# Optimization experiments

Measured on AMD Instinct MI355X. Metric: run time of the kernel, lower is better.

The kernel has to match this reference:

```python
import jax, jax.numpy as jnp
import numpy as np

N_CG_ITERS = 100


def _conv_same(x, k):
    # x: [C,H,W], k: [kh,kw]; depthwise cross-correlation, zero padding ('same')
    C = x.shape[0]
    rhs = jnp.broadcast_to(k, (C, 1) + k.shape)  # [C,1,kh,kw]
    return jax.lax.conv_general_dilated(
        x[None], rhs, window_strides=(1, 1), padding='SAME',
        dimension_numbers=('NCHW', 'OIHW', 'NCHW'),
        feature_group_count=C)[0]


def _flip(k):
    return k[::-1, ::-1]


def _apply_A(p, kernel, wsq, reg_kernels):
    # A = K^T K + sum_i w_i^2 G_i^T G_i
    KtKp = _conv_same(_conv_same(p, kernel), _flip(kernel))
    def one_reg(g):
        return _conv_same(_conv_same(p, g), _flip(g))
    reg = jax.vmap(one_reg)(reg_kernels)  # [n_reg, C, H, W]
    return KtKp + jnp.einsum('n,nchw->chw', wsq, reg)


def setup_inputs() -> dict:
    key = jax.random.key(0)
    k1, k2, k3, k4 = jax.random.split(key, 4)
    image = jax.random.uniform(k1, (3, 512, 512), dtype=jnp.float32)
    kernel = jax.random.uniform(k2, (11, 11), dtype=jnp.float32)
    kernel = kernel / jnp.sum(kernel)  # normalized blur PSF
    reg_kernels = 0.01 * jax.random.normal(k3, (2, 3, 3), dtype=jnp.float32)
    reg_kernel_weights = 1.0 + 0.01 * jax.random.normal(k4, (2,), dtype=jnp.float32)
    return {'image': image, 'kernel': kernel,
            'reg_kernel_weights': reg_kernel_weights, 'reg_kernels': reg_kernels}


def reference(image, kernel, reg_kernel_weights, reg_kernels):
    wsq = reg_kernel_weights * reg_kernel_weights
    # CG init: b = K^T * image, x0 = image, r0 = b - A x0, p0 = r0
    b = _conv_same(image, _flip(kernel))
    x0 = image
    r0 = b - _apply_A(x0, kernel, wsq, reg_kernels)
    p0 = r0

    def cg_step(carry, _):
        x, r, p = carry
        Ap = _apply_A(p, kernel, wsq, reg_kernels)
        rTr = jnp.sum(r * r)
        alpha = rTr / jnp.sum(p * Ap)
        x_new = x + alpha * p
        r_new = r - alpha * Ap
        beta = jnp.sum(r_new * r_new) / rTr
        p_new = r_new + beta * p
        return (x_new, r_new, p_new), None

    (x, r, p), _ = jax.lax.scan(cg_step, (x0, r0, p0), None, length=N_CG_ITERS)
    return x  # xrp[0] -> solved image [C,H,W]
```

## Files before the change

kernel.cpp:

```cpp
#include <hip/hip_runtime.h>


static constexpr int H = 512, W = 512, CCH = 3;
static constexpr int TDIM = 64;
static constexpr int RAD = 5;
static constexpr int HALO = 10;
static constexpr int PR = TDIM + 2 * HALO;
static constexpr int PSTR = 84;
static constexpr int TR = TDIM + 2 * RAD;
static constexpr int TSTR = 76;
static constexpr int NBLK = CCH * 8 * 8;
static constexpr int NTHR = 512;
static constexpr int NITER = 100;
static constexpr int FRN = 2960;
static constexpr int SPN = 2160;

__device__ __forceinline__ void load18(const float* __restrict__ row, float* __restrict__ v)
{
    const float4 a = *reinterpret_cast<const float4*>(row + 0);
    const float4 b = *reinterpret_cast<const float4*>(row + 4);
    const float4 c = *reinterpret_cast<const float4*>(row + 8);
    const float4 d = *reinterpret_cast<const float4*>(row + 12);
    const float2 e = *reinterpret_cast<const float2*>(row + 16);
    v[0]=a.x; v[1]=a.y; v[2]=a.z; v[3]=a.w;
    v[4]=b.x; v[5]=b.y; v[6]=b.z; v[7]=b.w;
    v[8]=c.x; v[9]=c.y; v[10]=c.z; v[11]=c.w;
    v[12]=d.x; v[13]=d.y; v[14]=d.z; v[15]=d.w;
    v[16]=e.x; v[17]=e.y;
}

__device__ __forceinline__ float block_reduce0(float v, float* red, int tid)
{
    __syncthreads();
    #pragma unroll
    for (int m = 32; m; m >>= 1) v += __shfl_xor(v, m, 64);
    if ((tid & 63) == 0) red[tid >> 6] = v;
    __syncthreads();
    float s = 0.f;
    if (tid == 0) {
        #pragma unroll
        for (int i = 0; i < NTHR / 64; ++i) s += red[i];
    }
    return s;
}

__device__ __forceinline__ float allreduce_bar(unsigned long long* slots, unsigned seq,
                                               float thread_partial,
                                               float* red, float* bc, int tid, int bid)
{
    float part = block_reduce0(thread_partial, red, tid);
    asm volatile("s_waitcnt vmcnt(0)" ::: "memory");
    __syncthreads();
    unsigned long long* buf = slots + (size_t)(seq & 1u) * 256;
    if (tid == 0) {
        unsigned long long u = ((unsigned long long)seq << 32)
                             | (unsigned long long)__float_as_uint(part);
        __hip_atomic_store(&buf[bid], u, __ATOMIC_RELAXED, __HIP_MEMORY_SCOPE_AGENT);
    }
    float mine = 0.f;
    if (tid < NBLK) {
        unsigned long long v;
        for (;;) {
            v = __hip_atomic_load(&buf[tid], __ATOMIC_RELAXED, __HIP_MEMORY_SCOPE_AGENT);
            if ((unsigned)(v >> 32) == seq) break;
            __builtin_amdgcn_s_sleep(1);
        }
        mine = __uint_as_float((unsigned)v);
    }
    float s = block_reduce0(mine, red, tid);
    if (tid == 0) *bc = s;
    __syncthreads();
    return *bc;
}

__device__ __forceinline__ void conv_fwd_phase(const float* __restrict__ kern,
                                               const float* __restrict__ P_,
                                               float* __restrict__ T_,
                                               int by0, int bx0, int tid)
{
    for (int seg = tid; seg < TR * 10; seg += NTHR) {
        int chunk = seg / TR;
        int ry    = seg - chunk * TR;
        int rx0   = chunk << 3;
        int gy    = by0 - RAD + ry;
        bool rowIn = (gy >= 0 && gy < H);
        float acc[8];
        #pragma unroll
        for (int j = 0; j < 8; ++j) acc[j] = 0.f;
        for (int a = 0; a < 11; ++a) {
            float v[18];
            load18(P_ + (ry + a) * PSTR + rx0, v);
            #pragma unroll
            for (int b = 0; b < 11; ++b) {
                float kw = kern[a * 11 + b];
                #pragma unroll
                for (int j = 0; j < 8; ++j) acc[j] = fmaf(v[b + j], kw, acc[j]);
            }
        }
        #pragma unroll
        for (int j = 0; j < 8; ++j) {
            int gx = bx0 - RAD + rx0 + j;
            bool in = rowIn && gx >= 0 && gx < W;
            acc[j] = in ? acc[j] : 0.f;
        }
        float* dst = T_ + ry * TSTR + rx0;
        if (rx0 < 72) {
            *reinterpret_cast<float4*>(dst)     = make_float4(acc[0], acc[1], acc[2], acc[3]);
            *reinterpret_cast<float4*>(dst + 4) = make_float4(acc[4], acc[5], acc[6], acc[7]);
        } else {
            dst[0] = acc[0];
            dst[1] = acc[1];
        }
    }
}

__device__ __forceinline__ void conv11_flip_acc_v(const float* __restrict__ src, int stride,
                                                  int row0, int col0,
                                                  const float* __restrict__ kern,
                                                  float acc[8])
{
    for (int a = 0; a < 11; ++a) {
        float v[18];
        load18(src + (row0 + a) * stride + col0, v);
        #pragma unroll
        for (int b = 0; b < 11; ++b) {
            float kw = kern[(10 - a) * 11 + (10 - b)];
            #pragma unroll
            for (int j = 0; j < 8; ++j) acc[j] = fmaf(v[b + j], kw, acc[j]);
        }
    }
}

__device__ __forceinline__ void conv11_flip_acc_s(const float* __restrict__ src, int stride,
                                                  int row0, int col0,
                                                  const float* __restrict__ kern,
                                                  float acc[8])
{
    for (int a = 0; a < 11; ++a) {
        const float* row = src + (row0 + a) * stride + col0;
        float v[18];
        #pragma unroll
        for (int b = 0; b < 18; ++b) v[b] = row[b];
        #pragma unroll
        for (int b = 0; b < 11; ++b) {
            float kw = kern[(10 - a) * 11 + (10 - b)];
            #pragma unroll
            for (int j = 0; j < 8; ++j) acc[j] = fmaf(v[b + j], kw, acc[j]);
        }
    }
}

__device__ __forceinline__ void reg_acc(const float* __restrict__ P_,
                                        const float* __restrict__ CB_,
                                        const float* __restrict__ gk,
                                        float w0sq, float w1sq,
                                        int oy, int ox0, int gy, int gx0,
                                        float acc[8])
{
    bool interior = (gy >= 1 && gy < H - 1 && gx0 >= 1 && gx0 <= W - 9);
    if (interior) {
        for (int a = 0; a < 5; ++a) {
            const float* row = P_ + (oy + 8 + a) * PSTR + ox0 + 8;
            const float4 q0 = *reinterpret_cast<const float4*>(row);
            const float4 q1 = *reinterpret_cast<const float4*>(row + 4);
            const float4 q2 = *reinterpret_cast<const float4*>(row + 8);
            float v[12] = {q0.x,q0.y,q0.z,q0.w, q1.x,q1.y,q1.z,q1.w, q2.x,q2.y,q2.z,q2.w};
            #pragma unroll
            for (int b = 0; b < 5; ++b) {
                float cb = CB_[a * 5 + b];
                #pragma unroll
                for (int j = 0; j < 8; ++j) acc[j] = fmaf(v[b + j], cb, acc[j]);
            }
        }
    } else {
        for (int j = 0; j < 8; ++j) {
            int gx = gx0 + j;
            float racc = 0.f;
            for (int dy = -1; dy <= 1; ++dy)
                for (int dx = -1; dx <= 1; ++dx) {
                    int qy = gy + dy, qx = gx + dx;
                    if (qy >= 0 && qy < H && qx >= 0 && qx < W) {
                        float u0 = 0.f, u1 = 0.f;
                        int pr0 = oy + 10 + dy - 1, pc0 = ox0 + j + 10 + dx - 1;
                        for (int sy = 0; sy < 3; ++sy)
                            for (int sx = 0; sx < 3; ++sx) {
                                float pv = P_[(pr0 + sy) * PSTR + pc0 + sx];
                                u0 = fmaf(pv, gk[sy * 3 + sx], u0);
                                u1 = fmaf(pv, gk[9 + sy * 3 + sx], u1);
                            }
                        racc += w0sq * gk[(1 - dy) * 3 + (1 - dx)] * u0
                              + w1sq * gk[9 + (1 - dy) * 3 + (1 - dx)] * u1;
                    }
                }
            acc[j] += racc;
        }
    }
}

__global__ void slot_init(unsigned long long* slots) { slots[threadIdx.x] = 0ull; }

__global__ void __launch_bounds__(NTHR)
__attribute__((amdgpu_waves_per_eu(2, 2)))
deconv_cg(const float* __restrict__ img, const float* __restrict__ kern,
          const float* __restrict__ wts, const float* __restrict__ gk,
          float* __restrict__ out, float* __restrict__ ws)
{
    asm volatile("" ::: "v255");

    __shared__ alignas(16) float P[PR * PSTR + 8];
    __shared__ alignas(16) float T[TR * TSTR + 8];
    __shared__ float CB[25];
    __shared__ float red[NTHR / 64];
    __shared__ float bc;

    const int tid = threadIdx.x;
    const int bid = blockIdx.x;
    const int ch  = bid / 64;
    const int tt  = bid - ch * 64;
    const int by0 = (tt >> 3) * TDIM;
    const int bx0 = (tt & 7) * TDIM;

    const float* imgc = img + ch * H * W;
    unsigned long long* slots = (unsigned long long*)ws;
    float* Hc = ws + 1024 + (size_t)ch * H * W;

    const float w0 = wts[0], w1 = wts[1];
    const float w0sq = w0 * w0, w1sq = w1 * w1;

    if (tid < 25) {
        int ty = tid / 5 - 2, tx = tid % 5 - 2;
        float s = 0.f;
        for (int ay = 0; ay < 3; ++ay)
            for (int ax = 0; ax < 3; ++ax) {
                int by_ = ay + ty, bx_ = ax + tx;
                if (by_ >= 0 && by_ < 3 && bx_ >= 0 && bx_ < 3)
                    s += w0sq * gk[ay * 3 + ax] * gk[by_ * 3 + bx_]
                       + w1sq * gk[9 + ay * 3 + ax] * gk[9 + by_ * 3 + bx_];
            }
        CB[tid] = s;
    }

    const int oy  = tid & 63;
    const int ox0 = (tid >> 6) << 3;
    const int gy  = by0 + oy;
    const int gx0 = bx0 + ox0;

    int fP[6], fG[6];
    #pragma unroll
    for (int k = 0; k < 6; ++k) {
        int idx = tid + k * NTHR;
        fP[k] = -1; fG[k] = -1;
        if (idx < FRN) {
            int py, px;
            if (idx < 840)       { py = idx / 84;              px = idx - py * 84; }
            else if (idx < 1680) { int t = idx - 840;  py = 74 + t / 84; px = t - (t / 84) * 84; }
            else                 { int t = idx - 1680; py = 10 + t / 20;
                                   int c = t - (t / 20) * 20;  px = (c < 10) ? c : (c + 64); }
            int iy = by0 - HALO + py, ix = bx0 - HALO + px;
            if (iy >= 0 && iy < H && ix >= 0 && ix < W) {
                fP[k] = py * PSTR + px;
                fG[k] = iy * W + ix;
            }
        }
    }
    int pT[5], pG[5];
    #pragma unroll
    for (int k = 0; k < 5; ++k) {
        int idx = tid + k * NTHR;
        pT[k] = -1; pG[k] = 0;
        if (idx < SPN) {
            int sy, sx;
            if (idx < 640)       { sy = idx >> 6;              sx = idx & 63; }
            else if (idx < 1280) { int t = idx - 640;  sy = 54 + (t >> 6); sx = t & 63; }
            else                 { int t = idx - 1280; sy = 10 + t / 20;
                                   int c = t - (t / 20) * 20;  sx = (c < 10) ? c : (c + 44); }
            pT[k] = sy * TSTR + sx;
            pG[k] = (by0 + sy) * W + bx0 + sx;
        }
    }

    float xr[8], rr[8], pr[8];

    for (int idx = tid; idx < PR * PR; idx += NTHR) {
        int py = idx / PR, px = idx - py * PR;
        int iy = by0 - HALO + py, ix = bx0 - HALO + px;
        float v = 0.f;
        if (iy >= 0 && iy < H && ix >= 0 && ix < W) v = imgc[iy * W + ix];
        P[py * PSTR + px] = v;
    }
    __syncthreads();
    conv_fwd_phase(kern, P, T, by0, bx0, tid);
    __syncthreads();
    float rTr, beta = 0.f;
    {
        float accA[8], accB[8];
        #pragma unroll
        for (int j = 0; j < 8; ++j) { accA[j] = 0.f; accB[j] = 0.f; }
        conv11_flip_acc_v(T, TSTR, oy, ox0, kern, accA);
        conv11_flip_acc_s(P, PSTR, oy + 5, ox0 + 5, kern, accB);
        reg_acc(P, CB, gk, w0sq, w1sq, oy, ox0, gy, gx0, accA);
        float dr = 0.f;
        #pragma unroll
        for (int j = 0; j < 8; ++j) {
            float r0 = accB[j] - accA[j];
            rr[j] = r0;  pr[j] = r0;
            xr[j] = P[(oy + HALO) * PSTR + ox0 + HALO + j];
            dr = fmaf(r0, r0, dr);
        }
        __syncthreads();
        float* st = T + oy * TSTR + ox0;
        *reinterpret_cast<float4*>(st)     = make_float4(rr[0], rr[1], rr[2], rr[3]);
        *reinterpret_cast<float4*>(st + 4) = make_float4(rr[4], rr[5], rr[6], rr[7]);
        __syncthreads();
        #pragma unroll
        for (int k = 0; k < 5; ++k)
            if (pT[k] >= 0)
                __hip_atomic_store(&Hc[pG[k]], T[pT[k]],
                                   __ATOMIC_RELAXED, __HIP_MEMORY_SCOPE_AGENT);
        rTr = allreduce_bar(slots, 1u, dr, red, &bc, tid, bid);
    }

    for (int it = 0; it < NITER; ++it) {
        #pragma unroll
        for (int j = 0; j < 8; ++j) pr[j] = fmaf(beta, pr[j], rr[j]);
        float fv[6];
        #pragma unroll
        for (int k = 0; k < 6; ++k)
            fv[k] = (fG[k] >= 0)
                  ? __hip_atomic_load(&Hc[fG[k]], __ATOMIC_RELAXED, __HIP_MEMORY_SCOPE_AGENT)
                  : 0.f;
        #pragma unroll
        for (int k = 0; k < 6; ++k)
            if (fG[k] >= 0)
                P[fP[k]] = fmaf(beta, P[fP[k]], fv[k]);
        {
            float* ow = P + (oy + HALO) * PSTR + ox0 + HALO;
            *reinterpret_cast<float2*>(ow)     = make_float2(pr[0], pr[1]);
            *reinterpret_cast<float2*>(ow + 2) = make_float2(pr[2], pr[3]);
            *reinterpret_cast<float2*>(ow + 4) = make_float2(pr[4], pr[5]);
            *reinterpret_cast<float2*>(ow + 6) = make_float2(pr[6], pr[7]);
        }
        __syncthreads();

        conv_fwd_phase(kern, P, T, by0, bx0, tid);
        __syncthreads();

        float Ap[8];
        float dp = 0.f;
        {
            float acc[8];
            #pragma unroll
            for (int j = 0; j < 8; ++j) acc[j] = 0.f;
            conv11_flip_acc_v(T, TSTR, oy, ox0, kern, acc);
            reg_acc(P, CB, gk, w0sq, w1sq, oy, ox0, gy, gx0, acc);
            #pragma unroll
            for (int j = 0; j < 8; ++j) {
                Ap[j] = acc[j];
                dp = fmaf(pr[j], Ap[j], dp);
            }
        }
        float pAp   = allreduce_bar(slots, 2u * it + 2u, dp, red, &bc, tid, bid);
        float alpha = rTr / pAp;

        float dr = 0.f;
        #pragma unroll
        for (int j = 0; j < 8; ++j) {
            xr[j] = fmaf(alpha, pr[j], xr[j]);
            rr[j] = fmaf(-alpha, Ap[j], rr[j]);
            dr = fmaf(rr[j], rr[j], dr);
        }
        {
            float* st = T + oy * TSTR + ox0;
            *reinterpret_cast<float4*>(st)     = make_float4(rr[0], rr[1], rr[2], rr[3]);
            *reinterpret_cast<float4*>(st + 4) = make_float4(rr[4], rr[5], rr[6], rr[7]);
        }
        __syncthreads();
        #pragma unroll
        for (int k = 0; k < 5; ++k)
            if (pT[k] >= 0)
                __hip_atomic_store(&Hc[pG[k]], T[pT[k]],
                                   __ATOMIC_RELAXED, __HIP_MEMORY_SCOPE_AGENT);
        float s = allreduce_bar(slots, 2u * it + 3u, dr, red, &bc, tid, bid);
        beta = s / rTr;
        rTr  = s;
    }

    float* op = out + ch * H * W + gy * W + gx0;
    *reinterpret_cast<float4*>(op)     = make_float4(xr[0], xr[1], xr[2], xr[3]);
    *reinterpret_cast<float4*>(op + 4) = make_float4(xr[4], xr[5], xr[6], xr[7]);
}

extern "C" void kernel_launch(void* const* d_in, const int* in_sizes, int n_in,
                              void* d_out, int out_size, void* d_ws, size_t ws_size,
                              hipStream_t stream)
{
    (void)in_sizes; (void)n_in; (void)out_size; (void)ws_size;
    const float* img  = (const float*)d_in[0];
    const float* kern = (const float*)d_in[1];
    const float* wts  = (const float*)d_in[2];
    const float* gk   = (const float*)d_in[3];
    float* out = (float*)d_out;
    float* ws  = (float*)d_ws;

    slot_init<<<1, 512, 0, stream>>>((unsigned long long*)ws);
    deconv_cg<<<dim3(NBLK), dim3(NTHR), 0, stream>>>(img, kern, wts, gk, out, ws);
}
```

Baseline: 4.711 ms.

## Switch to Chronopoulos-Gear single-reduction CG with fused two-value grid allreduce

```diff
diff --git a/kernel.cpp b/kernel.cpp
--- a/kernel.cpp
+++ b/kernel.cpp
@@ -29,46 +29,57 @@
     v[16]=e.x; v[17]=e.y;
 }
 
-__device__ __forceinline__ float block_reduce0(float v, float* red, int tid)
+__device__ __forceinline__ float2 allreduce2_bar(unsigned long long* slots, unsigned seq,
+                                                 float va, float vb,
+                                                 float* redA, float* redB, float2* bc,
+                                                 int tid, int bid)
 {
     __syncthreads();
     #pragma unroll
-    for (int m = 32; m; m >>= 1) v += __shfl_xor(v, m, 64);
-    if ((tid & 63) == 0) red[tid >> 6] = v;
-    __syncthreads();
-    float s = 0.f;
+    for (int m = 32; m; m >>= 1) { va += __shfl_xor(va, m, 64); vb += __shfl_xor(vb, m, 64); }
+    if ((tid & 63) == 0) { redA[tid >> 6] = va; redB[tid >> 6] = vb; }
+    asm volatile("s_waitcnt vmcnt(0)" ::: "memory");
+    __syncthreads();
+    unsigned long long* bufA = slots + (size_t)(seq & 1u) * 512;
+    unsigned long long* bufB = bufA + 256;
     if (tid == 0) {
-        #pragma unroll
-        for (int i = 0; i < NTHR / 64; ++i) s += red[i];
-    }
-    return s;
-}
-
-__device__ __forceinline__ float allreduce_bar(unsigned long long* slots, unsigned seq,
-                                               float thread_partial,
-                                               float* red, float* bc, int tid, int bid)
-{
-    float part = block_reduce0(thread_partial, red, tid);
-    asm volatile("s_waitcnt vmcnt(0)" ::: "memory");
-    __syncthreads();
-    unsigned long long* buf = slots + (size_t)(seq & 1u) * 256;
-    if (tid == 0) {
-        unsigned long long u = ((unsigned long long)seq << 32)
-                             | (unsigned long long)__float_as_uint(part);
-        __hip_atomic_store(&buf[bid], u, __ATOMIC_RELAXED, __HIP_MEMORY_SCOPE_AGENT);
-    }
-    float mine = 0.f;
+        float sa = 0.f, sb = 0.f;
+        #pragma unroll
+        for (int i = 0; i < NTHR / 64; ++i) { sa += redA[i]; sb += redB[i]; }
+        __hip_atomic_store(&bufA[bid],
+            ((unsigned long long)seq << 32) | (unsigned long long)__float_as_uint(sa),
+            __ATOMIC_RELAXED, __HIP_MEMORY_SCOPE_AGENT);
+        __hip_atomic_store(&bufB[bid],
+            ((unsigned long long)seq << 32) | (unsigned long long)__float_as_uint(sb),
+            __ATOMIC_RELAXED, __HIP_MEMORY_SCOPE_AGENT);
+    }
+    float ma = 0.f, mb = 0.f;
     if (tid < NBLK) {
         unsigned long long v;
         for (;;) {
-            v = __hip_atomic_load(&buf[tid], __ATOMIC_RELAXED, __HIP_MEMORY_SCOPE_AGENT);
+            v = __hip_atomic_load(&bufA[tid], __ATOMIC_RELAXED, __HIP_MEMORY_SCOPE_AGENT);
             if ((unsigned)(v >> 32) == seq) break;
             __builtin_amdgcn_s_sleep(1);
         }
-        mine = __uint_as_float((unsigned)v);
-    }
-    float s = block_reduce0(mine, red, tid);
-    if (tid == 0) *bc = s;
+        ma = __uint_as_float((unsigned)v);
+        for (;;) {
+            v = __hip_atomic_load(&bufB[tid], __ATOMIC_RELAXED, __HIP_MEMORY_SCOPE_AGENT);
+            if ((unsigned)(v >> 32) == seq) break;
+            __builtin_amdgcn_s_sleep(1);
+        }
+        mb = __uint_as_float((unsigned)v);
+    }
+    __syncthreads();
+    #pragma unroll
+    for (int m = 32; m; m >>= 1) { ma += __shfl_xor(ma, m, 64); mb += __shfl_xor(mb, m, 64); }
+    if ((tid & 63) == 0) { redA[tid >> 6] = ma; redB[tid >> 6] = mb; }
+    __syncthreads();
+    if (tid == 0) {
+        float sa = 0.f, sb = 0.f;
+        #pragma unroll
+        for (int i = 0; i < NTHR / 64; ++i) { sa += redA[i]; sb += redB[i]; }
+        bc->x = sa; bc->y = sb;
+    }
     __syncthreads();
     return *bc;
 }
@@ -150,49 +161,47 @@
     }
 }
 
-__device__ __forceinline__ void reg_acc(const float* __restrict__ P_,
-                                        const float* __restrict__ CB_,
-                                        const float* __restrict__ gk,
-                                        float w0sq, float w1sq,
-                                        int oy, int ox0, int gy, int gx0,
-                                        float acc[8])
-{
-    bool interior = (gy >= 1 && gy < H - 1 && gx0 >= 1 && gx0 <= W - 9);
-    if (interior) {
-        for (int a = 0; a < 5; ++a) {
-            const float* row = P_ + (oy + 8 + a) * PSTR + ox0 + 8;
-            const float4 q0 = *reinterpret_cast<const float4*>(row);
-            const float4 q1 = *reinterpret_cast<const float4*>(row + 4);
-            const float4 q2 = *reinterpret_cast<const float4*>(row + 8);
-            float v[12] = {q0.x,q0.y,q0.z,q0.w, q1.x,q1.y,q1.z,q1.w, q2.x,q2.y,q2.z,q2.w};
-            #pragma unroll
-            for (int b = 0; b < 5; ++b) {
-                float cb = CB_[a * 5 + b];
-                #pragma unroll
-                for (int j = 0; j < 8; ++j) acc[j] = fmaf(v[b + j], cb, acc[j]);
-            }
-        }
-    } else {
+__device__ __forceinline__ void reg_uniform(const float* __restrict__ P_,
+                                            const float* __restrict__ CB_,
+                                            const float* __restrict__ gk,
+                                            float w0sq, float w1sq,
+                                            int oy, int ox0, int gy, int gx0,
+                                            float acc[8])
+{
+    for (int a = 0; a < 5; ++a) {
+        const float* row = P_ + (oy + 8 + a) * PSTR + ox0 + 8;
+        const float4 q0 = *reinterpret_cast<const float4*>(row);
+        const float4 q1 = *reinterpret_cast<const float4*>(row + 4);
+        const float4 q2 = *reinterpret_cast<const float4*>(row + 8);
+        float v[12] = {q0.x,q0.y,q0.z,q0.w, q1.x,q1.y,q1.z,q1.w, q2.x,q2.y,q2.z,q2.w};
+        #pragma unroll
+        for (int b = 0; b < 5; ++b) {
+            float cb = CB_[a * 5 + b];
+            #pragma unroll
+            for (int j = 0; j < 8; ++j) acc[j] = fmaf(v[b + j], cb, acc[j]);
+        }
+    }
+    if (!(gy > 0 && gy < H - 1 && gx0 > 0 && gx0 + 7 < W - 1)) {
         for (int j = 0; j < 8; ++j) {
             int gx = gx0 + j;
-            float racc = 0.f;
+            if (gy > 0 && gy < H - 1 && gx > 0 && gx < W - 1) continue;
+            float corr = 0.f;
             for (int dy = -1; dy <= 1; ++dy)
                 for (int dx = -1; dx <= 1; ++dx) {
                     int qy = gy + dy, qx = gx + dx;
-                    if (qy >= 0 && qy < H && qx >= 0 && qx < W) {
-                        float u0 = 0.f, u1 = 0.f;
-                        int pr0 = oy + 10 + dy - 1, pc0 = ox0 + j + 10 + dx - 1;
-                        for (int sy = 0; sy < 3; ++sy)
-                            for (int sx = 0; sx < 3; ++sx) {
-                                float pv = P_[(pr0 + sy) * PSTR + pc0 + sx];
-                                u0 = fmaf(pv, gk[sy * 3 + sx], u0);
-                                u1 = fmaf(pv, gk[9 + sy * 3 + sx], u1);
-                            }
-                        racc += w0sq * gk[(1 - dy) * 3 + (1 - dx)] * u0
-                              + w1sq * gk[9 + (1 - dy) * 3 + (1 - dx)] * u1;
-                    }
+                    if (qy >= 0 && qy < H && qx >= 0 && qx < W) continue;
+                    float u0 = 0.f, u1 = 0.f;
+                    int pr0 = oy + HALO + dy - 1, pc0 = ox0 + j + HALO + dx - 1;
+                    for (int sy = 0; sy < 3; ++sy)
+                        for (int sx = 0; sx < 3; ++sx) {
+                            float pv = P_[(pr0 + sy) * PSTR + pc0 + sx];
+                            u0 = fmaf(pv, gk[sy * 3 + sx], u0);
+                            u1 = fmaf(pv, gk[9 + sy * 3 + sx], u1);
+                        }
+                    corr += w0sq * gk[(1 - dy) * 3 + (1 - dx)] * u0
+                          + w1sq * gk[9 + (1 - dy) * 3 + (1 - dx)] * u1;
                 }
-            acc[j] += racc;
+            acc[j] -= corr;
         }
     }
 }
@@ -200,18 +209,16 @@
 __global__ void slot_init(unsigned long long* slots) { slots[threadIdx.x] = 0ull; }
 
 __global__ void __launch_bounds__(NTHR)
-__attribute__((amdgpu_waves_per_eu(2, 2)))
 deconv_cg(const float* __restrict__ img, const float* __restrict__ kern,
           const float* __restrict__ wts, const float* __restrict__ gk,
           float* __restrict__ out, float* __restrict__ ws)
 {
-    asm volatile("" ::: "v255");
-
     __shared__ alignas(16) float P[PR * PSTR + 8];
     __shared__ alignas(16) float T[TR * TSTR + 8];
+    __shared__ float Sf[FRN];
     __shared__ float CB[25];
-    __shared__ float red[NTHR / 64];
-    __shared__ float bc;
+    __shared__ float redA[NTHR / 64], redB[NTHR / 64];
+    __shared__ float2 bc2;
 
     const int tid = threadIdx.x;
     const int bid = blockIdx.x;
@@ -222,7 +229,7 @@
 
     const float* imgc = img + ch * H * W;
     unsigned long long* slots = (unsigned long long*)ws;
-    float* Hc = ws + 1024 + (size_t)ch * H * W;
+    float* Hc = ws + 2048 + (size_t)ch * H * W;
 
     const float w0 = wts[0], w1 = wts[1];
     const float w0sq = w0 * w0, w1sq = w1 * w1;
@@ -245,11 +252,11 @@
     const int gy  = by0 + oy;
     const int gx0 = bx0 + ox0;
 
-    int fP[6], fG[6];
+    int fP[6], fG[6], fS[6];
     #pragma unroll
     for (int k = 0; k < 6; ++k) {
         int idx = tid + k * NTHR;
-        fP[k] = -1; fG[k] = -1;
+        fP[k] = -1; fG[k] = -1; fS[k] = idx;
         if (idx < FRN) {
             int py, px;
             if (idx < 840)       { py = idx / 84;              px = idx - py * 84; }
@@ -279,7 +286,10 @@
         }
     }
 
-    float xr[8], rr[8], pr[8];
+    float xr[8], rr[8], pr[8], sr[8];
+    #pragma unroll
+    for (int j = 0; j < 8; ++j) { pr[j] = 0.f; sr[j] = 0.f; }
+    for (int idx = tid; idx < FRN; idx += NTHR) Sf[idx] = 0.f;
 
     for (int idx = tid; idx < PR * PR; idx += NTHR) {
         int py = idx / PR, px = idx - py * PR;
@@ -291,21 +301,17 @@
     __syncthreads();
     conv_fwd_phase(kern, P, T, by0, bx0, tid);
     __syncthreads();
-    float rTr, beta = 0.f;
     {
         float accA[8], accB[8];
         #pragma unroll
         for (int j = 0; j < 8; ++j) { accA[j] = 0.f; accB[j] = 0.f; }
         conv11_flip_acc_v(T, TSTR, oy, ox0, kern, accA);
         conv11_flip_acc_s(P, PSTR, oy + 5, ox0 + 5, kern, accB);
-        reg_acc(P, CB, gk, w0sq, w1sq, oy, ox0, gy, gx0, accA);
-        float dr = 0.f;
+        reg_uniform(P, CB, gk, w0sq, w1sq, oy, ox0, gy, gx0, accA);
         #pragma unroll
         for (int j = 0; j < 8; ++j) {
-            float r0 = accB[j] - accA[j];
-            rr[j] = r0;  pr[j] = r0;
+            rr[j] = accB[j] - accA[j];
             xr[j] = P[(oy + HALO) * PSTR + ox0 + HALO + j];
-            dr = fmaf(r0, r0, dr);
         }
         __syncthreads();
         float* st = T + oy * TSTR + ox0;
@@ -317,72 +323,88 @@
             if (pT[k] >= 0)
                 __hip_atomic_store(&Hc[pG[k]], T[pT[k]],
                                    __ATOMIC_RELAXED, __HIP_MEMORY_SCOPE_AGENT);
-        rTr = allreduce_bar(slots, 1u, dr, red, &bc, tid, bid);
-    }
-
-    for (int it = 0; it < NITER; ++it) {
-        #pragma unroll
-        for (int j = 0; j < 8; ++j) pr[j] = fmaf(beta, pr[j], rr[j]);
-        float fv[6];
-        #pragma unroll
-        for (int k = 0; k < 6; ++k)
-            fv[k] = (fG[k] >= 0)
-                  ? __hip_atomic_load(&Hc[fG[k]], __ATOMIC_RELAXED, __HIP_MEMORY_SCOPE_AGENT)
-                  : 0.f;
+        (void)allreduce2_bar(slots, 1u, 0.f, 0.f, redA, redB, &bc2, tid, bid);
         #pragma unroll
         for (int k = 0; k < 6; ++k)
             if (fG[k] >= 0)
-                P[fP[k]] = fmaf(beta, P[fP[k]], fv[k]);
-        {
-            float* ow = P + (oy + HALO) * PSTR + ox0 + HALO;
-            *reinterpret_cast<float2*>(ow)     = make_float2(pr[0], pr[1]);
-            *reinterpret_cast<float2*>(ow + 2) = make_float2(pr[2], pr[3]);
-            *reinterpret_cast<float2*>(ow + 4) = make_float2(pr[4], pr[5]);
-            *reinterpret_cast<float2*>(ow + 6) = make_float2(pr[6], pr[7]);
-        }
+                P[fP[k]] = __hip_atomic_load(&Hc[fG[k]],
+                                             __ATOMIC_RELAXED, __HIP_MEMORY_SCOPE_AGENT);
+        float* ow = P + (oy + HALO) * PSTR + ox0 + HALO;
+        *reinterpret_cast<float2*>(ow)     = make_float2(rr[0], rr[1]);
+        *reinterpret_cast<float2*>(ow + 2) = make_float2(rr[2], rr[3]);
+        *reinterpret_cast<float2*>(ow + 4) = make_float2(rr[4], rr[5]);
+        *reinterpret_cast<float2*>(ow + 6) = make_float2(rr[6], rr[7]);
+    }
+
+    float gamma_old = 1.f, alpha_old = 1.f;
+
+    for (int it = 0; it < NITER; ++it) {
         __syncthreads();
 
         conv_fwd_phase(kern, P, T, by0, bx0, tid);
         __syncthreads();
-
-        float Ap[8];
-        float dp = 0.f;
+        float wv[8];
+        float ga = 0.f, de = 0.f;
         {
             float acc[8];
             #pragma unroll
             for (int j = 0; j < 8; ++j) acc[j] = 0.f;
             conv11_flip_acc_v(T, TSTR, oy, ox0, kern, acc);
-            reg_acc(P, CB, gk, w0sq, w1sq, oy, ox0, gy, gx0, acc);
+            reg_uniform(P, CB, gk, w0sq, w1sq, oy, ox0, gy, gx0, acc);
             #pragma unroll
             for (int j = 0; j < 8; ++j) {
-                Ap[j] = acc[j];
-                dp = fmaf(pr[j], Ap[j], dp);
+                wv[j] = acc[j];
+                ga = fmaf(rr[j], rr[j], ga);
+                de = fmaf(rr[j], wv[j], de);
             }
         }
-        float pAp   = allreduce_bar(slots, 2u * it + 2u, dp, red, &bc, tid, bid);
-        float alpha = rTr / pAp;
-
-        float dr = 0.f;
-        #pragma unroll
-        for (int j = 0; j < 8; ++j) {
-            xr[j] = fmaf(alpha, pr[j], xr[j]);
-            rr[j] = fmaf(-alpha, Ap[j], rr[j]);
-            dr = fmaf(rr[j], rr[j], dr);
-        }
-        {
-            float* st = T + oy * TSTR + ox0;
-            *reinterpret_cast<float4*>(st)     = make_float4(rr[0], rr[1], rr[2], rr[3]);
-            *reinterpret_cast<float4*>(st + 4) = make_float4(rr[4], rr[5], rr[6], rr[7]);
-        }
+        __syncthreads();
+        float* st = T + oy * TSTR + ox0;
+        *reinterpret_cast<float4*>(st)     = make_float4(wv[0], wv[1], wv[2], wv[3]);
+        *reinterpret_cast<float4*>(st + 4) = make_float4(wv[4], wv[5], wv[6], wv[7]);
         __syncthreads();
         #pragma unroll
         for (int k = 0; k < 5; ++k)
             if (pT[k] >= 0)
                 __hip_atomic_store(&Hc[pG[k]], T[pT[k]],
                                    __ATOMIC_RELAXED, __HIP_MEMORY_SCOPE_AGENT);
-        float s = allreduce_bar(slots, 2u * it + 3u, dr, red, &bc, tid, bid);
-        beta = s / rTr;
-        rTr  = s;
+
+        float2 gd = allreduce2_bar(slots, (unsigned)(it + 2), ga, de,
+                                   redA, redB, &bc2, tid, bid);
+        float gamma = gd.x, delta = gd.y;
+        float beta  = (it == 0) ? 0.f : gamma / gamma_old;
+        float alpha = (it == 0) ? gamma / delta
+                                : gamma / (delta - beta * gamma / alpha_old);
+
+        float wf[6];
+        #pragma unroll
+        for (int k = 0; k < 6; ++k)
+            wf[k] = (fG[k] >= 0)
+                  ? __hip_atomic_load(&Hc[fG[k]], __ATOMIC_RELAXED, __HIP_MEMORY_SCOPE_AGENT)
+                  : 0.f;
+
+        #pragma unroll
+        for (int j = 0; j < 8; ++j) {
+            pr[j] = fmaf(beta, pr[j], rr[j]);
+            sr[j] = fmaf(beta, sr[j], wv[j]);
+            xr[j] = fmaf(alpha, pr[j], xr[j]);
+            rr[j] = fmaf(-alpha, sr[j], rr[j]);
+        }
+        #pragma unroll
+        for (int k = 0; k < 6; ++k)
+            if (fG[k] >= 0) {
+                float s = fmaf(beta, Sf[fS[k]], wf[k]);
+                Sf[fS[k]] = s;
+                P[fP[k]]  = fmaf(-alpha, s, P[fP[k]]);
+            }
+        float* ow = P + (oy + HALO) * PSTR + ox0 + HALO;
+        *reinterpret_cast<float2*>(ow)     = make_float2(rr[0], rr[1]);
+        *reinterpret_cast<float2*>(ow + 2) = make_float2(rr[2], rr[3]);
+        *reinterpret_cast<float2*>(ow + 4) = make_float2(rr[4], rr[5]);
+        *reinterpret_cast<float2*>(ow + 6) = make_float2(rr[6], rr[7]);
+
+        gamma_old = gamma;
+        alpha_old = alpha;
     }
 
     float* op = out + ch * H * W + gy * W + gx0;
@@ -402,6 +424,6 @@
     float* out = (float*)d_out;
     float* ws  = (float*)d_ws;
 
-    slot_init<<<1, 512, 0, stream>>>((unsigned long long*)ws);
+    slot_init<<<1, 1024, 0, stream>>>((unsigned long long*)ws);
     deconv_cg<<<dim3(NBLK), dim3(NTHR), 0, stream>>>(img, kern, wts, gk, out, ws);
 }
```

New measurement: 4.207 ms. 10.7% less time.
